# Kernel optimization log

Measured on AMD Instinct MI355X. Metric: run time of the kernel, lower is better.

The kernel has to match this reference:

```python
import jax, jax.numpy as jnp
import numpy as np

N = 50000
E = 800000
IN_FEATS = 256
OUT_FEATS = 128
NEG_SLOPE = 0.2
ALPHA = 0.5


def segment_softmax(x, seg, num_segments):
    # numerically-stable softmax over edges grouped by destination node
    m = jax.ops.segment_max(x, seg, num_segments=num_segments)
    z = jnp.exp(x - m[seg])
    s = jax.ops.segment_sum(z, seg, num_segments=num_segments)
    return z / s[seg]


def setup_inputs() -> dict:
    key = jax.random.key(0)
    ks = jax.random.split(key, 8)
    feat = jax.random.normal(ks[0], (N, IN_FEATS), dtype=jnp.float32)
    w = jax.random.normal(ks[1], (E,), dtype=jnp.float32)
    fc_w = jax.random.normal(ks[2], (IN_FEATS, OUT_FEATS), dtype=jnp.float32) * (1.0 / np.sqrt(IN_FEATS))
    attn_l = jax.random.normal(ks[3], (1, 1, OUT_FEATS), dtype=jnp.float32) * 0.1
    attn_r = jax.random.normal(ks[4], (1, 1, OUT_FEATS), dtype=jnp.float32) * 0.1
    bias_param = jnp.zeros((OUT_FEATS,), dtype=jnp.float32)
    src = jax.random.randint(ks[5], (E,), 0, N, dtype=jnp.int32)
    dst = jax.random.randint(ks[6], (E,), 0, N, dtype=jnp.int32)
    return {"feat": feat, "w": w, "fc_w": fc_w, "attn_l": attn_l,
            "attn_r": attn_r, "bias_param": bias_param, "src": src, "dst": dst}


def reference(feat, w, fc_w, attn_l, attn_r, bias_param, src, dst):
    # fc projection: [N, H=1, D]
    ft = (feat @ fc_w).reshape(N, 1, OUT_FEATS)
    # per-node attention logits [N, 1]
    el = (ft * attn_l).sum(-1)
    er = (ft * attn_r).sum(-1)
    # u_add_v edge scores + leaky relu: [E, 1]
    e = el[src] + er[dst]
    e = jnp.where(e > 0, e, NEG_SLOPE * e)
    # edge_softmax over destination neighborhoods (per head); H==1 so squeeze to [E]
    a = segment_softmax(e[:, 0], dst, N)
    # edge_softmax of precomputed edge weight 'w'
    ws = segment_softmax(w, dst, N)
    # blend attentions
    a = a * (1.0 - ALPHA) + ws * ALPHA
    # u_mul_e + sum aggregation: [E,1,D] messages -> [N,1,D]
    m = ft[src] * a[:, None, None]
    rst = jax.ops.segment_sum(m, dst, num_segments=N)
    rst = rst + bias_param.reshape(1, 1, OUT_FEATS)
    return rst
```

## Files before the change

kernel.cpp:

```cpp
#include <hip/hip_runtime.h>

#define NN 50000
#define NE 800000
#define KIN 256
#define DOUT 128
#define NEG_SLOPE 0.2f
#define ALPHA 0.5f
#define ELL_CAP 48

#define RSH 9
#define RSZ 512
#define NREG ((NN + RSZ - 1) / RSZ)
#define RCAP 9216
#define EPB 8192
#define NAB ((NE + EPB - 1) / EPB)

#define GEMM_BLKS ((NN + 63) / 64)

typedef __attribute__((ext_vector_type(8))) short bf16x8;
typedef __attribute__((ext_vector_type(4))) float f32x4;

__device__ __forceinline__ unsigned short f2b(float v) {
  unsigned int u = __float_as_uint(v);
  return (unsigned short)((u + 0x7fffu + ((u >> 16) & 1u)) >> 16);
}
__device__ __forceinline__ float b2f(unsigned short h) {
  return __uint_as_float(((unsigned int)h) << 16);
}
__device__ __forceinline__ unsigned short f2h(float v) {
  _Float16 h = (_Float16)v;
  return __builtin_bit_cast(unsigned short, h);
}
__device__ __forceinline__ float h2f(unsigned short u) {
  return (float)__builtin_bit_cast(_Float16, u);
}

__global__ void prep_b(const float* __restrict__ fc_w, unsigned short* __restrict__ b_hi,
                       unsigned short* __restrict__ b_lo) {
  int t = blockIdx.x * 256 + threadIdx.x;
  if (t >= KIN * DOUT) return;
  int k = t >> 7, c = t & 127;
  float v = fc_w[t];
  unsigned short h = f2b(v);
  unsigned short l = f2b(v - b2f(h));
  int kt = k >> 5, kl = k & 31;
  int g = kl >> 3, j = kl & 7;
  int idx = ((kt * 128 + c) * 4 + g) * 8 + j;
  b_hi[idx] = h;
  b_lo[idx] = l;
}

__global__ __launch_bounds__(256) void pass_a(
    const int* __restrict__ src, const int* __restrict__ dst,
    const float* __restrict__ w, int* __restrict__ gcur, uint2* __restrict__ ebuf) {
  __shared__ int hist[NREG];
  __shared__ int cu[NREG];
  const int tid = threadIdx.x, b = blockIdx.x;
  for (int i = tid; i < NREG; i += 256) hist[i] = 0;
  __syncthreads();
  const int base = b * EPB;
#pragma unroll
  for (int it = 0; it < EPB / 1024; ++it) {
    int e = base + it * 1024 + tid * 4;
    if (e < NE) {
      int4 d4 = *(const int4*)(dst + e);
      atomicAdd(&hist[d4.x >> RSH], 1);
      atomicAdd(&hist[d4.y >> RSH], 1);
      atomicAdd(&hist[d4.z >> RSH], 1);
      atomicAdd(&hist[d4.w >> RSH], 1);
    }
  }
  __syncthreads();
  if (tid < NREG) cu[tid] = atomicAdd(&gcur[tid], hist[tid]);
  __syncthreads();
#pragma unroll
  for (int it = 0; it < EPB / 1024; ++it) {
    int e = base + it * 1024 + tid * 4;
    if (e < NE) {
      int4 s4 = *(const int4*)(src + e);
      int4 d4 = *(const int4*)(dst + e);
      float4 w4 = *(const float4*)(w + e);
      int r0 = d4.x >> RSH, r1 = d4.y >> RSH, r2 = d4.z >> RSH, r3 = d4.w >> RSH;
      int o0 = atomicAdd(&cu[r0], 1);
      int o1 = atomicAdd(&cu[r1], 1);
      int o2 = atomicAdd(&cu[r2], 1);
      int o3 = atomicAdd(&cu[r3], 1);
      if (o0 < RCAP) ebuf[r0 * RCAP + o0] = make_uint2(((unsigned)s4.x << 16) | f2h(w4.x), d4.x & (RSZ - 1));
      if (o1 < RCAP) ebuf[r1 * RCAP + o1] = make_uint2(((unsigned)s4.y << 16) | f2h(w4.y), d4.y & (RSZ - 1));
      if (o2 < RCAP) ebuf[r2 * RCAP + o2] = make_uint2(((unsigned)s4.z << 16) | f2h(w4.z), d4.z & (RSZ - 1));
      if (o3 < RCAP) ebuf[r3 * RCAP + o3] = make_uint2(((unsigned)s4.w << 16) | f2h(w4.w), d4.w & (RSZ - 1));
    }
  }
}

__global__ __launch_bounds__(256) void passb_gemm(
    const int* __restrict__ gcur, const uint2* __restrict__ ebuf,
    unsigned int* __restrict__ ell, int* __restrict__ deg,
    const float* __restrict__ feat, const unsigned short* __restrict__ b_hi,
    const unsigned short* __restrict__ b_lo, const float* __restrict__ attn_l,
    const float* __restrict__ attn_r, unsigned short* __restrict__ ft16,
    float* __restrict__ el, float* __restrict__ er) {
  const int tid = threadIdx.x;

  if (blockIdx.x < NREG) {
    __shared__ int cnt[RSZ];
    const int r = blockIdx.x;
    for (int i = tid; i < RSZ; i += 256) cnt[i] = 0;
    __syncthreads();
    const int c = min(gcur[r], RCAP);
    const uint2* rb = ebuf + (size_t)r * RCAP;
    for (int i = tid; i < c; i += 256) {
      uint2 en = rb[i];
      int p = atomicAdd(&cnt[en.y], 1);
      if (p < ELL_CAP)
        ell[(size_t)((r << RSH) + en.y) * ELL_CAP + p] = en.x;
    }
    __syncthreads();
    for (int i = tid; i < RSZ; i += 256) {
      int n = (r << RSH) + i;
      if (n < NN) deg[n] = cnt[i];
    }
    return;
  }

  const int q = blockIdx.x - NREG;
  const int lane = tid & 63;
  const int wv = tid >> 6;
  const int cl = lane & 15;
  const int g = lane >> 4;
  const int row = q * 64 + wv * 16 + cl;
  const size_t arow = (size_t)min(row, NN - 1) * KIN;
  const int boff0 = cl * 32 + g * 8;

  float4 abuf[16];
#pragma unroll
  for (int kt = 0; kt < 8; ++kt) {
    const float* ap = feat + arow + kt * 32 + g * 8;
    abuf[2 * kt] = *(const float4*)ap;
    abuf[2 * kt + 1] = *(const float4*)(ap + 4);
  }

  f32x4 acc[8];
#pragma unroll
  for (int ct = 0; ct < 8; ++ct) acc[ct] = (f32x4){0.f, 0.f, 0.f, 0.f};

#pragma unroll
  for (int kt = 0; kt < 8; ++kt) {
    float4 a0 = abuf[2 * kt];
    float4 a1 = abuf[2 * kt + 1];
    bf16x8 ah, alo;
    {
      float f[8] = {a0.x, a0.y, a0.z, a0.w, a1.x, a1.y, a1.z, a1.w};
#pragma unroll
      for (int j = 0; j < 8; ++j) {
        unsigned short h = f2b(f[j]);
        ah[j] = (short)h;
        alo[j] = (short)f2b(f[j] - b2f(h));
      }
    }
    const unsigned short* bh = b_hi + kt * 4096 + boff0;
    const unsigned short* bl = b_lo + kt * 4096 + boff0;
#pragma unroll
    for (int ct = 0; ct < 8; ++ct) {
      bf16x8 bhv = *(const bf16x8*)(bh + ct * 512);
      bf16x8 blv = *(const bf16x8*)(bl + ct * 512);
      acc[ct] = __builtin_amdgcn_mfma_f32_16x16x32_bf16(ah, bhv, acc[ct], 0, 0, 0);
      acc[ct] = __builtin_amdgcn_mfma_f32_16x16x32_bf16(alo, bhv, acc[ct], 0, 0, 0);
      acc[ct] = __builtin_amdgcn_mfma_f32_16x16x32_bf16(ah, blv, acc[ct], 0, 0, 0);
    }
  }

  float pl[4] = {0, 0, 0, 0}, pr[4] = {0, 0, 0, 0};
  const int r0 = q * 64 + wv * 16 + g * 4;
#pragma unroll
  for (int ct = 0; ct < 8; ++ct) {
    int col = ct * 16 + cl;
    float av = attn_l[col];
    float bv = attn_r[col];
#pragma unroll
    for (int qq = 0; qq < 4; ++qq) {
      float v = acc[ct][qq];
      int rr = r0 + qq;
      if (rr < NN) ft16[(size_t)rr * DOUT + col] = f2b(v);
      pl[qq] = fmaf(v, av, pl[qq]);
      pr[qq] = fmaf(v, bv, pr[qq]);
    }
  }
#pragma unroll
  for (int qq = 0; qq < 4; ++qq) {
    float a = pl[qq], b = pr[qq];
#pragma unroll
    for (int d = 1; d < 16; d <<= 1) {
      a += __shfl_xor(a, d);
      b += __shfl_xor(b, d);
    }
    if (cl == 0) {
      int rr = r0 + qq;
      if (rr < NN) { el[rr] = a; er[rr] = b; }
    }
  }
}

__global__ __launch_bounds__(256) void agg(
    const unsigned short* __restrict__ ft16, const unsigned int* __restrict__ ell,
    const int* __restrict__ deg, const float* __restrict__ el,
    const float* __restrict__ er, const float* __restrict__ bias,
    float* __restrict__ out) {
  const int lane = threadIdx.x & 63;
  const int wv = threadIdx.x >> 6;
  const int n = blockIdx.x * 4 + wv;
  if (n >= NN) return;
  const int dg = min(deg[n], ELL_CAP);
  const float ern = er[n];

  float z = 0.f, zw = 0.f;
  int so = 0;
  if (lane < dg) {
    unsigned u = ell[(size_t)n * ELL_CAP + lane];
    int s = (int)(u >> 16);
    so = s * DOUT;
    float x = el[s] + ern;
    x = (x > 0.f) ? x : NEG_SLOPE * x;
    z = __expf(x);
    zw = __expf(h2f((unsigned short)(u & 0xffffu)));
  }
  float se = z, sw = zw;
#pragma unroll
  for (int d = 1; d < 64; d <<= 1) {
    se += __shfl_xor(se, d);
    sw += __shfl_xor(sw, d);
  }
  const float coef = z * ((1.f - ALPHA) / se) + zw * (ALPHA / sw);

  float acc[8] = {0.f, 0.f, 0.f, 0.f, 0.f, 0.f, 0.f, 0.f};
  const unsigned short* ftp = ft16 + (lane & 15) * 8;
  const int lg = lane >> 4;
  for (int jb = 0; jb < dg; jb += 16) {
    int j0 = jb + lg;
    float c0 = __shfl(coef, j0), c1 = __shfl(coef, j0 + 4);
    float c2 = __shfl(coef, j0 + 8), c3 = __shfl(coef, j0 + 12);
    int s0 = __shfl(so, j0), s1 = __shfl(so, j0 + 4);
    int s2 = __shfl(so, j0 + 8), s3 = __shfl(so, j0 + 12);
    bf16x8 r0 = *(const bf16x8*)(ftp + s0);
    bf16x8 r1 = *(const bf16x8*)(ftp + s1);
    bf16x8 r2 = *(const bf16x8*)(ftp + s2);
    bf16x8 r3 = *(const bf16x8*)(ftp + s3);
#pragma unroll
    for (int c = 0; c < 8; ++c) {
      acc[c] = fmaf(c0, b2f((unsigned short)r0[c]), acc[c]);
      acc[c] = fmaf(c1, b2f((unsigned short)r1[c]), acc[c]);
      acc[c] = fmaf(c2, b2f((unsigned short)r2[c]), acc[c]);
      acc[c] = fmaf(c3, b2f((unsigned short)r3[c]), acc[c]);
    }
  }
#pragma unroll
  for (int c = 0; c < 8; ++c) {
    acc[c] += __shfl_xor(acc[c], 16);
    acc[c] += __shfl_xor(acc[c], 32);
  }
  if (lane < 16) {
    const float4 b0 = *(const float4*)(bias + lane * 8);
    const float4 b1 = *(const float4*)(bias + lane * 8 + 4);
    float4 o0, o1;
    o0.x = acc[0] + b0.x; o0.y = acc[1] + b0.y; o0.z = acc[2] + b0.z; o0.w = acc[3] + b0.w;
    o1.x = acc[4] + b1.x; o1.y = acc[5] + b1.y; o1.z = acc[6] + b1.z; o1.w = acc[7] + b1.w;
    float* op = out + (size_t)n * DOUT + lane * 8;
    *(float4*)op = o0;
    *(float4*)(op + 4) = o1;
  }
}

extern "C" void kernel_launch(void* const* d_in, const int* in_sizes, int n_in,
                              void* d_out, int out_size, void* d_ws, size_t ws_size,
                              hipStream_t stream) {
  const float* feat = (const float*)d_in[0];
  const float* w = (const float*)d_in[1];
  const float* fc_w = (const float*)d_in[2];
  const float* attn_l = (const float*)d_in[3];
  const float* attn_r = (const float*)d_in[4];
  const float* bias = (const float*)d_in[5];
  const int* src = (const int*)d_in[6];
  const int* dst = (const int*)d_in[7];
  float* out = (float*)d_out;

  char* ws = (char*)d_ws;
  size_t o = 0;
  auto take = [&](size_t bytes) {
    char* p = ws + o;
    o = (o + bytes + 255) & ~(size_t)255;
    return p;
  };
  unsigned short* ft16 = (unsigned short*)take((size_t)NN * DOUT * 2);
  float* el = (float*)take((size_t)NN * 4);
  float* er = (float*)take((size_t)NN * 4);
  unsigned short* b_hi = (unsigned short*)take((size_t)KIN * DOUT * 2);
  unsigned short* b_lo = (unsigned short*)take((size_t)KIN * DOUT * 2);
  int* gcur = (int*)take((size_t)NREG * 4);
  int* deg = (int*)take((size_t)NN * 4);
  uint2* ebuf = (uint2*)take((size_t)NREG * RCAP * 8);
  unsigned int* ell = (unsigned int*)take((size_t)(NREG * RSZ) * ELL_CAP * 4);

  hipMemsetAsync(gcur, 0, (size_t)NREG * 4, stream);
  prep_b<<<(KIN * DOUT + 255) / 256, 256, 0, stream>>>(fc_w, b_hi, b_lo);
  pass_a<<<NAB, 256, 0, stream>>>(src, dst, w, gcur, ebuf);
  passb_gemm<<<NREG + GEMM_BLKS, 256, 0, stream>>>(gcur, ebuf, ell, deg, feat, b_hi, b_lo,
                                                   attn_l, attn_r, ft16, el, er);
  agg<<<(NN + 3) / 4, 256, 0, stream>>>(ft16, ell, deg, el, er, bias, out);
}
```

Before: 192.4 us.

## Fuse all stages into one cooperative persistent kernel with grid syncs

Replaces the four separate launches with a single cooperative persistent kernel that loops over virtual blocks per stage and separates the stages with grid-wide syncs. Non-cooperative fused kernels remain as a fallback. The GEMM now loads A one k-tile ahead instead of preloading everything, and the aggregation unrolls gathers to eight rows per step based on degree. The aim is to remove launch gaps and tails between kernels. The cost is grid-sync overhead, a persistent grid capped by occupancy and by launch_bounds(256,4), and possible register pressure.

```diff
diff --git a/kernel.cpp b/kernel.cpp
--- a/kernel.cpp
+++ b/kernel.cpp
@@ -1,4 +1,7 @@
 #include <hip/hip_runtime.h>
+#include <hip/hip_cooperative_groups.h>
+
+namespace cg = cooperative_groups;
 
 #define NN 50000
 #define NE 800000
@@ -15,7 +18,10 @@
 #define EPB 8192
 #define NAB ((NE + EPB - 1) / EPB)
 
+#define PREP_BLKS ((KIN * DOUT + 255) / 256)
 #define GEMM_BLKS ((NN + 63) / 64)
+#define AGG_BLKS ((NN + 3) / 4)
+#define NUM_CU 256
 
 typedef __attribute__((ext_vector_type(8))) short bf16x8;
 typedef __attribute__((ext_vector_type(4))) float f32x4;
@@ -35,28 +41,30 @@
   return (float)__builtin_bit_cast(_Float16, u);
 }
 
-__global__ void prep_b(const float* __restrict__ fc_w, unsigned short* __restrict__ b_hi,
-                       unsigned short* __restrict__ b_lo) {
-  int t = blockIdx.x * 256 + threadIdx.x;
-  if (t >= KIN * DOUT) return;
-  int k = t >> 7, c = t & 127;
-  float v = fc_w[t];
-  unsigned short h = f2b(v);
-  unsigned short l = f2b(v - b2f(h));
-  int kt = k >> 5, kl = k & 31;
-  int g = kl >> 3, j = kl & 7;
-  int idx = ((kt * 128 + c) * 4 + g) * 8 + j;
-  b_hi[idx] = h;
-  b_lo[idx] = l;
-}
-
-__global__ __launch_bounds__(256) void pass_a(
-    const int* __restrict__ src, const int* __restrict__ dst,
-    const float* __restrict__ w, int* __restrict__ gcur, uint2* __restrict__ ebuf) {
-  __shared__ int hist[NREG];
-  __shared__ int cu[NREG];
-  const int tid = threadIdx.x, b = blockIdx.x;
-  for (int i = tid; i < NREG; i += 256) hist[i] = 0;
+
+__device__ __forceinline__ void do_prep(int vb, int tid, const float* __restrict__ fc_w,
+                                        unsigned short* __restrict__ b_hi,
+                                        unsigned short* __restrict__ b_lo) {
+  int t = vb * 256 + tid;
+  if (t < KIN * DOUT) {
+    int k = t >> 7, c = t & 127;
+    float v = fc_w[t];
+    unsigned short h = f2b(v);
+    unsigned short l = f2b(v - b2f(h));
+    int kt = k >> 5, kl = k & 31;
+    int g = kl >> 3, j = kl & 7;
+    int idx = ((kt * 128 + c) * 4 + g) * 8 + j;
+    b_hi[idx] = h;
+    b_lo[idx] = l;
+  }
+}
+
+__device__ __forceinline__ void do_passa(int b, int tid, const int* __restrict__ src,
+                                         const int* __restrict__ dst,
+                                         const float* __restrict__ w,
+                                         int* __restrict__ gcur, uint2* __restrict__ ebuf,
+                                         int* sh_hist, int* sh_cu) {
+  for (int i = tid; i < NREG; i += 256) sh_hist[i] = 0;
   __syncthreads();
   const int base = b * EPB;
 #pragma unroll
@@ -64,14 +72,14 @@
     int e = base + it * 1024 + tid * 4;
     if (e < NE) {
       int4 d4 = *(const int4*)(dst + e);
-      atomicAdd(&hist[d4.x >> RSH], 1);
-      atomicAdd(&hist[d4.y >> RSH], 1);
-      atomicAdd(&hist[d4.z >> RSH], 1);
-      atomicAdd(&hist[d4.w >> RSH], 1);
-    }
-  }
-  __syncthreads();
-  if (tid < NREG) cu[tid] = atomicAdd(&gcur[tid], hist[tid]);
+      atomicAdd(&sh_hist[d4.x >> RSH], 1);
+      atomicAdd(&sh_hist[d4.y >> RSH], 1);
+      atomicAdd(&sh_hist[d4.z >> RSH], 1);
+      atomicAdd(&sh_hist[d4.w >> RSH], 1);
+    }
+  }
+  __syncthreads();
+  if (tid < NREG) sh_cu[tid] = atomicAdd(&gcur[tid], sh_hist[tid]);
   __syncthreads();
 #pragma unroll
   for (int it = 0; it < EPB / 1024; ++it) {
@@ -81,76 +89,72 @@
       int4 d4 = *(const int4*)(dst + e);
       float4 w4 = *(const float4*)(w + e);
       int r0 = d4.x >> RSH, r1 = d4.y >> RSH, r2 = d4.z >> RSH, r3 = d4.w >> RSH;
-      int o0 = atomicAdd(&cu[r0], 1);
-      int o1 = atomicAdd(&cu[r1], 1);
-      int o2 = atomicAdd(&cu[r2], 1);
-      int o3 = atomicAdd(&cu[r3], 1);
+      int o0 = atomicAdd(&sh_cu[r0], 1);
+      int o1 = atomicAdd(&sh_cu[r1], 1);
+      int o2 = atomicAdd(&sh_cu[r2], 1);
+      int o3 = atomicAdd(&sh_cu[r3], 1);
       if (o0 < RCAP) ebuf[r0 * RCAP + o0] = make_uint2(((unsigned)s4.x << 16) | f2h(w4.x), d4.x & (RSZ - 1));
       if (o1 < RCAP) ebuf[r1 * RCAP + o1] = make_uint2(((unsigned)s4.y << 16) | f2h(w4.y), d4.y & (RSZ - 1));
       if (o2 < RCAP) ebuf[r2 * RCAP + o2] = make_uint2(((unsigned)s4.z << 16) | f2h(w4.z), d4.z & (RSZ - 1));
       if (o3 < RCAP) ebuf[r3 * RCAP + o3] = make_uint2(((unsigned)s4.w << 16) | f2h(w4.w), d4.w & (RSZ - 1));
     }
   }
-}
-
-__global__ __launch_bounds__(256) void passb_gemm(
-    const int* __restrict__ gcur, const uint2* __restrict__ ebuf,
-    unsigned int* __restrict__ ell, int* __restrict__ deg,
-    const float* __restrict__ feat, const unsigned short* __restrict__ b_hi,
-    const unsigned short* __restrict__ b_lo, const float* __restrict__ attn_l,
-    const float* __restrict__ attn_r, unsigned short* __restrict__ ft16,
-    float* __restrict__ el, float* __restrict__ er) {
-  const int tid = threadIdx.x;
-
-  if (blockIdx.x < NREG) {
-    __shared__ int cnt[RSZ];
-    const int r = blockIdx.x;
-    for (int i = tid; i < RSZ; i += 256) cnt[i] = 0;
-    __syncthreads();
-    const int c = min(gcur[r], RCAP);
-    const uint2* rb = ebuf + (size_t)r * RCAP;
-    for (int i = tid; i < c; i += 256) {
-      uint2 en = rb[i];
-      int p = atomicAdd(&cnt[en.y], 1);
-      if (p < ELL_CAP)
-        ell[(size_t)((r << RSH) + en.y) * ELL_CAP + p] = en.x;
-    }
-    __syncthreads();
-    for (int i = tid; i < RSZ; i += 256) {
-      int n = (r << RSH) + i;
-      if (n < NN) deg[n] = cnt[i];
-    }
-    return;
-  }
-
-  const int q = blockIdx.x - NREG;
+  __syncthreads();
+}
+
+__device__ __forceinline__ void do_passb(int r, int tid, const int* __restrict__ gcur,
+                                         const uint2* __restrict__ ebuf,
+                                         unsigned int* __restrict__ ell,
+                                         int* __restrict__ deg, int* sh_cnt) {
+  for (int i = tid; i < RSZ; i += 256) sh_cnt[i] = 0;
+  __syncthreads();
+  const int c = min(gcur[r], RCAP);
+  const uint2* rb = ebuf + (size_t)r * RCAP;
+  for (int i = tid; i < c; i += 256) {
+    uint2 en = rb[i];
+    int p = atomicAdd(&sh_cnt[en.y], 1);
+    if (p < ELL_CAP)
+      ell[(size_t)((r << RSH) + en.y) * ELL_CAP + p] = en.x;
+  }
+  __syncthreads();
+  for (int i = tid; i < RSZ; i += 256) {
+    int n = (r << RSH) + i;
+    if (n < NN) deg[n] = sh_cnt[i];
+  }
+  __syncthreads();
+}
+
+__device__ __forceinline__ void do_gemm(int q, int tid, const float* __restrict__ feat,
+                                        const unsigned short* __restrict__ b_hi,
+                                        const unsigned short* __restrict__ b_lo,
+                                        const float* __restrict__ attn_l,
+                                        const float* __restrict__ attn_r,
+                                        unsigned short* __restrict__ ft16,
+                                        float* __restrict__ el, float* __restrict__ er) {
   const int lane = tid & 63;
   const int wv = tid >> 6;
   const int cl = lane & 15;
   const int g = lane >> 4;
   const int row = q * 64 + wv * 16 + cl;
-  const size_t arow = (size_t)min(row, NN - 1) * KIN;
+  const float* ap = feat + (size_t)min(row, NN - 1) * KIN + g * 8;
   const int boff0 = cl * 32 + g * 8;
 
-  float4 abuf[16];
+  f32x4 acc[8];
+#pragma unroll
+  for (int ct = 0; ct < 8; ++ct) acc[ct] = (f32x4){0.f, 0.f, 0.f, 0.f};
+
+  float4 pa0 = *(const float4*)ap;
+  float4 pa1 = *(const float4*)(ap + 4);
 #pragma unroll
   for (int kt = 0; kt < 8; ++kt) {
-    const float* ap = feat + arow + kt * 32 + g * 8;
-    abuf[2 * kt] = *(const float4*)ap;
-    abuf[2 * kt + 1] = *(const float4*)(ap + 4);
-  }
-
-  f32x4 acc[8];
-#pragma unroll
-  for (int ct = 0; ct < 8; ++ct) acc[ct] = (f32x4){0.f, 0.f, 0.f, 0.f};
-
-#pragma unroll
-  for (int kt = 0; kt < 8; ++kt) {
-    float4 a0 = abuf[2 * kt];
-    float4 a1 = abuf[2 * kt + 1];
+    float4 na0, na1;
+    if (kt < 7) {
+      na0 = *(const float4*)(ap + (kt + 1) * 32);
+      na1 = *(const float4*)(ap + (kt + 1) * 32 + 4);
+    }
     bf16x8 ah, alo;
     {
-      float f[8] = {a0.x, a0.y, a0.z, a0.w, a1.x, a1.y, a1.z, a1.w};
+      float f[8] = {pa0.x, pa0.y, pa0.z, pa0.w, pa1.x, pa1.y, pa1.z, pa1.w};
 #pragma unroll
       for (int j = 0; j < 8; ++j) {
         unsigned short h = f2b(f[j]);
@@ -168,6 +172,8 @@
       acc[ct] = __builtin_amdgcn_mfma_f32_16x16x32_bf16(alo, bhv, acc[ct], 0, 0, 0);
       acc[ct] = __builtin_amdgcn_mfma_f32_16x16x32_bf16(ah, blv, acc[ct], 0, 0, 0);
     }
+    pa0 = na0;
+    pa1 = na1;
   }
 
   float pl[4] = {0, 0, 0, 0}, pr[4] = {0, 0, 0, 0};
@@ -201,14 +207,16 @@
   }
 }
 
-__global__ __launch_bounds__(256) void agg(
-    const unsigned short* __restrict__ ft16, const unsigned int* __restrict__ ell,
-    const int* __restrict__ deg, const float* __restrict__ el,
-    const float* __restrict__ er, const float* __restrict__ bias,
-    float* __restrict__ out) {
-  const int lane = threadIdx.x & 63;
-  const int wv = threadIdx.x >> 6;
-  const int n = blockIdx.x * 4 + wv;
+__device__ __forceinline__ void do_agg(int vb, int tid, const unsigned short* __restrict__ ft16,
+                                       const unsigned int* __restrict__ ell,
+                                       const int* __restrict__ deg,
+                                       const float* __restrict__ el,
+                                       const float* __restrict__ er,
+                                       const float* __restrict__ bias,
+                                       float* __restrict__ out) {
+  const int lane = tid & 63;
+  const int wv = tid >> 6;
+  const int n = vb * 4 + wv;
   if (n >= NN) return;
   const int dg = min(deg[n], ELL_CAP);
   const float ern = er[n];
@@ -235,7 +243,8 @@
   float acc[8] = {0.f, 0.f, 0.f, 0.f, 0.f, 0.f, 0.f, 0.f};
   const unsigned short* ftp = ft16 + (lane & 15) * 8;
   const int lg = lane >> 4;
-  for (int jb = 0; jb < dg; jb += 16) {
+
+  auto g4 = [&](int jb) {
     int j0 = jb + lg;
     float c0 = __shfl(coef, j0), c1 = __shfl(coef, j0 + 4);
     float c2 = __shfl(coef, j0 + 8), c3 = __shfl(coef, j0 + 12);
@@ -252,7 +261,47 @@
       acc[c] = fmaf(c2, b2f((unsigned short)r2[c]), acc[c]);
       acc[c] = fmaf(c3, b2f((unsigned short)r3[c]), acc[c]);
     }
-  }
+  };
+  auto g8 = [&]() {
+    int j0 = lg;
+    float c0 = __shfl(coef, j0), c1 = __shfl(coef, j0 + 4);
+    float c2 = __shfl(coef, j0 + 8), c3 = __shfl(coef, j0 + 12);
+    float c4 = __shfl(coef, j0 + 16), c5 = __shfl(coef, j0 + 20);
+    float c6 = __shfl(coef, j0 + 24), c7 = __shfl(coef, j0 + 28);
+    int s0 = __shfl(so, j0), s1 = __shfl(so, j0 + 4);
+    int s2 = __shfl(so, j0 + 8), s3 = __shfl(so, j0 + 12);
+    int s4 = __shfl(so, j0 + 16), s5 = __shfl(so, j0 + 20);
+    int s6 = __shfl(so, j0 + 24), s7 = __shfl(so, j0 + 28);
+    bf16x8 r0 = *(const bf16x8*)(ftp + s0);
+    bf16x8 r1 = *(const bf16x8*)(ftp + s1);
+    bf16x8 r2 = *(const bf16x8*)(ftp + s2);
+    bf16x8 r3 = *(const bf16x8*)(ftp + s3);
+    bf16x8 r4 = *(const bf16x8*)(ftp + s4);
+    bf16x8 r5 = *(const bf16x8*)(ftp + s5);
+    bf16x8 r6 = *(const bf16x8*)(ftp + s6);
+    bf16x8 r7 = *(const bf16x8*)(ftp + s7);
+#pragma unroll
+    for (int c = 0; c < 8; ++c) {
+      acc[c] = fmaf(c0, b2f((unsigned short)r0[c]), acc[c]);
+      acc[c] = fmaf(c1, b2f((unsigned short)r1[c]), acc[c]);
+      acc[c] = fmaf(c2, b2f((unsigned short)r2[c]), acc[c]);
+      acc[c] = fmaf(c3, b2f((unsigned short)r3[c]), acc[c]);
+      acc[c] = fmaf(c4, b2f((unsigned short)r4[c]), acc[c]);
+      acc[c] = fmaf(c5, b2f((unsigned short)r5[c]), acc[c]);
+      acc[c] = fmaf(c6, b2f((unsigned short)r6[c]), acc[c]);
+      acc[c] = fmaf(c7, b2f((unsigned short)r7[c]), acc[c]);
+    }
+  };
+
+  if (dg <= 16) {
+    g4(0);
+  } else if (dg <= 32) {
+    g8();
+  } else {
+    g8();
+    g4(32);
+  }
+
 #pragma unroll
   for (int c = 0; c < 8; ++c) {
     acc[c] += __shfl_xor(acc[c], 16);
@@ -268,6 +317,67 @@
     *(float4*)op = o0;
     *(float4*)(op + 4) = o1;
   }
+}
+
+__global__ __launch_bounds__(256, 4) void mega(
+    const float* __restrict__ feat, const int* __restrict__ src,
+    const int* __restrict__ dst, const float* __restrict__ w,
+    const float* __restrict__ fc_w, const float* __restrict__ attn_l,
+    const float* __restrict__ attn_r, const float* __restrict__ bias,
+    float* __restrict__ out, unsigned short* __restrict__ ft16,
+    float* __restrict__ el, float* __restrict__ er,
+    unsigned short* __restrict__ b_hi, unsigned short* __restrict__ b_lo,
+    int* __restrict__ gcur, int* __restrict__ deg,
+    uint2* __restrict__ ebuf, unsigned int* __restrict__ ell) {
+  cg::grid_group grid = cg::this_grid();
+  __shared__ int sh_hist[NREG];
+  __shared__ int sh_cu[NREG];
+  __shared__ int sh_cnt[RSZ];
+  const int tid = threadIdx.x;
+
+  for (int vb = blockIdx.x; vb < PREP_BLKS + NAB; vb += gridDim.x) {
+    if (vb < PREP_BLKS) do_prep(vb, tid, fc_w, b_hi, b_lo);
+    else do_passa(vb - PREP_BLKS, tid, src, dst, w, gcur, ebuf, sh_hist, sh_cu);
+  }
+  grid.sync();
+  for (int vb = blockIdx.x; vb < NREG + GEMM_BLKS; vb += gridDim.x) {
+    if (vb < NREG) do_passb(vb, tid, gcur, ebuf, ell, deg, sh_cnt);
+    else do_gemm(vb - NREG, tid, feat, b_hi, b_lo, attn_l, attn_r, ft16, el, er);
+  }
+  grid.sync();
+  for (int vb = blockIdx.x; vb < AGG_BLKS; vb += gridDim.x)
+    do_agg(vb, tid, ft16, ell, deg, el, er, bias, out);
+}
+
+__global__ __launch_bounds__(256) void k_prep_passa(
+    const int* __restrict__ src, const int* __restrict__ dst,
+    const float* __restrict__ w, const float* __restrict__ fc_w,
+    unsigned short* __restrict__ b_hi, unsigned short* __restrict__ b_lo,
+    int* __restrict__ gcur, uint2* __restrict__ ebuf) {
+  __shared__ int sh_hist[NREG];
+  __shared__ int sh_cu[NREG];
+  if (blockIdx.x < PREP_BLKS) do_prep(blockIdx.x, threadIdx.x, fc_w, b_hi, b_lo);
+  else do_passa(blockIdx.x - PREP_BLKS, threadIdx.x, src, dst, w, gcur, ebuf, sh_hist, sh_cu);
+}
+
+__global__ __launch_bounds__(256) void k_passb_gemm(
+    const int* __restrict__ gcur, const uint2* __restrict__ ebuf,
+    unsigned int* __restrict__ ell, int* __restrict__ deg,
+    const float* __restrict__ feat, const unsigned short* __restrict__ b_hi,
+    const unsigned short* __restrict__ b_lo, const float* __restrict__ attn_l,
+    const float* __restrict__ attn_r, unsigned short* __restrict__ ft16,
+    float* __restrict__ el, float* __restrict__ er) {
+  __shared__ int sh_cnt[RSZ];
+  if (blockIdx.x < NREG) do_passb(blockIdx.x, threadIdx.x, gcur, ebuf, ell, deg, sh_cnt);
+  else do_gemm(blockIdx.x - NREG, threadIdx.x, feat, b_hi, b_lo, attn_l, attn_r, ft16, el, er);
+}
+
+__global__ __launch_bounds__(256) void k_agg(
+    const unsigned short* __restrict__ ft16, const unsigned int* __restrict__ ell,
+    const int* __restrict__ deg, const float* __restrict__ el,
+    const float* __restrict__ er, const float* __restrict__ bias,
+    float* __restrict__ out) {
+  do_agg(blockIdx.x, threadIdx.x, ft16, ell, deg, el, er, bias, out);
 }
 
 extern "C" void kernel_launch(void* const* d_in, const int* in_sizes, int n_in,
@@ -300,10 +410,25 @@
   uint2* ebuf = (uint2*)take((size_t)NREG * RCAP * 8);
   unsigned int* ell = (unsigned int*)take((size_t)(NREG * RSZ) * ELL_CAP * 4);
 
-  hipMemsetAsync(gcur, 0, (size_t)NREG * 4, stream);
-  prep_b<<<(KIN * DOUT + 255) / 256, 256, 0, stream>>>(fc_w, b_hi, b_lo);
-  pass_a<<<NAB, 256, 0, stream>>>(src, dst, w, gcur, ebuf);
-  passb_gemm<<<NREG + GEMM_BLKS, 256, 0, stream>>>(gcur, ebuf, ell, deg, feat, b_hi, b_lo,
-                                                   attn_l, attn_r, ft16, el, er);
-  agg<<<(NN + 3) / 4, 256, 0, stream>>>(ft16, ell, deg, el, er, bias, out);
-}
+  (void)hipMemsetAsync(gcur, 0, (size_t)NREG * 4, stream);
+
+  int maxPerCU = 0;
+  hipError_t qe = hipOccupancyMaxActiveBlocksPerMultiprocessor(
+      &maxPerCU, reinterpret_cast<const void*>(mega), 256, 0);
+  bool done = false;
+  if (qe == hipSuccess && maxPerCU >= 1) {
+    int nblk = maxPerCU * NUM_CU;
+    if (nblk > 2048) nblk = 2048;
+    void* args[] = {&feat, &src, &dst, &w, &fc_w, &attn_l, &attn_r, &bias, &out,
+                    &ft16, &el, &er, &b_hi, &b_lo, &gcur, &deg, &ebuf, &ell};
+    hipError_t le = hipLaunchCooperativeKernel(reinterpret_cast<void*>(mega),
+                                               dim3(nblk), dim3(256), args, 0, stream);
+    done = (le == hipSuccess);
+  }
+  if (!done) {
+    k_prep_passa<<<PREP_BLKS + NAB, 256, 0, stream>>>(src, dst, w, fc_w, b_hi, b_lo, gcur, ebuf);
+    k_passb_gemm<<<NREG + GEMM_BLKS, 256, 0, stream>>>(gcur, ebuf, ell, deg, feat, b_hi, b_lo,
+                                                       attn_l, attn_r, ft16, el, er);
+    k_agg<<<AGG_BLKS, 256, 0, stream>>>(ft16, ell, deg, el, er, bias, out);
+  }
+}
```

New measurement: 441.4 us. +129.4%, slower.
